# Kernel optimization log

Hardware: AMD Instinct MI355X
Metric: run time of the kernel (lower is better)

The kernel has to match this reference:

```python
import jax, jax.numpy as jnp
import numpy as np

N_NODES = 50000
N_EDGES = 800000
NUM_GRAPHS = 512
NEG_SLOPE = 0.2  # PyG GATv2Conv default negative_slope


def setup_inputs() -> dict:
    key = jax.random.key(0)
    ks = jax.random.split(key, 16)
    F_in, H = 128, 2
    C1, C2, NC = 32, 16, 6
    x = jax.random.normal(ks[0], (N_NODES, F_in), dtype=jnp.float32)
    edge_index = jax.random.randint(ks[1], (2, N_EDGES), 0, N_NODES, dtype=jnp.int64)
    batch = jnp.sort(jax.random.randint(ks[2], (N_NODES,), 0, NUM_GRAPHS, dtype=jnp.int64))
    s = lambda fan_in: 1.0 / np.sqrt(fan_in)
    return {
        "x": x, "edge_index": edge_index, "batch": batch,
        # conv1: in=128 -> heads=2, out=32 (concat 64)
        "Wl1": jax.random.normal(ks[3], (F_in, H * C1), jnp.float32) * s(F_in),
        "bl1": jnp.zeros((H * C1,), jnp.float32),
        "Wr1": jax.random.normal(ks[4], (F_in, H * C1), jnp.float32) * s(F_in),
        "att1": jax.random.normal(ks[5], (H, C1), jnp.float32) * s(C1),
        "b1": jnp.zeros((H * C1,), jnp.float32),
        # conv2: in=64 -> heads=2, out=16 (concat 32)
        "Wl2": jax.random.normal(ks[6], (H * C1, H * C2), jnp.float32) * s(H * C1),
        "bl2": jnp.zeros((H * C2,), jnp.float32),
        "Wr2": jax.random.normal(ks[7], (H * C1, H * C2), jnp.float32) * s(H * C1),
        "att2": jax.random.normal(ks[8], (H, C2), jnp.float32) * s(C2),
        "b2": jnp.zeros((H * C2,), jnp.float32),
        # fc: 32 -> 6
        "Wfc": jax.random.normal(ks[9], (H * C2, NC), jnp.float32) * s(H * C2),
        "bfc": jnp.zeros((NC,), jnp.float32),
    }


def _gatv2_conv(x, src, dst, Wl, bl, Wr, att, bias):
    """PyG GATv2Conv (concat heads, add_self_loops already applied to src/dst)."""
    H, C = att.shape
    N = x.shape[0]
    xl = (x @ Wl + bl).reshape(N, H, C)  # source/message transform
    xr = (x @ Wr).reshape(N, H, C)       # target transform
    e = jax.nn.leaky_relu(xl[src] + xr[dst], NEG_SLOPE)  # [E,H,C]
    score = jnp.einsum('ehc,hc->eh', e, att)             # [E,H]
    # segment softmax over edges sharing the same destination node
    smax = jax.ops.segment_max(score, dst, num_segments=N)      # [N,H]
    ex = jnp.exp(score - smax[dst])
    denom = jax.ops.segment_sum(ex, dst, num_segments=N)        # [N,H]
    alpha = ex / denom[dst]                                     # [E,H]
    out = jax.ops.segment_sum(alpha[:, :, None] * xl[src], dst, num_segments=N)
    return out.reshape(N, H * C) + bias


def reference(x, edge_index, batch, Wl1, bl1, Wr1, att1, b1,
              Wl2, bl2, Wr2, att2, b2, Wfc, bfc):
    N = x.shape[0]
    loops = jnp.arange(N, dtype=edge_index.dtype)
    src = jnp.concatenate([edge_index[0], loops])  # add_self_loops=True
    dst = jnp.concatenate([edge_index[1], loops])
    h = jax.nn.elu(_gatv2_conv(x, src, dst, Wl1, bl1, Wr1, att1, b1))
    h = jax.nn.elu(_gatv2_conv(h, src, dst, Wl2, bl2, Wr2, att2, b2))
    # global mean pool over graphs
    sums = jax.ops.segment_sum(h, batch, num_segments=NUM_GRAPHS)
    cnt = jax.ops.segment_sum(jnp.ones((N,), h.dtype), batch, num_segments=NUM_GRAPHS)
    pooled = sums / jnp.maximum(cnt, 1.0)[:, None]
    return jax.nn.log_softmax(pooled @ Wfc + bfc, axis=1)
```

## Files before the change

kernel.cpp:

```cpp
#include <hip/hip_runtime.h>
#include <math.h>

#define N_NODES 50000
#define N_EDGES 800000
#define NUM_GRAPHS 512
#define NEG_SLOPE 0.2f
#define LOG_MD 6
#define ROWCAP 63
#define NBKT 196
#define NPART 200
#define EPB_PART 4000

typedef unsigned short ushort_t;
typedef unsigned int   uint_t;
typedef __attribute__((ext_vector_type(4))) float f32x4;
typedef __attribute__((ext_vector_type(8))) short s16x8;

__device__ __forceinline__ ushort_t f2bf(float f) {
    union { float f; uint_t u; } v; v.f = f;
    uint_t u = v.u;
    return (ushort_t)((u + 0x7fffu + ((u >> 16) & 1u)) >> 16);
}

__global__ void hist_k(const int* __restrict__ ei_dst, int* __restrict__ bucket_cnt,
                       float* __restrict__ gz) {
    __shared__ int h[NBKT];
    const int tid = threadIdx.x;
    for (int i = tid; i < NBKT; i += 256) h[i] = 0;
    int gt = blockIdx.x * 256 + tid;
    if (gt < NUM_GRAPHS * 33) gz[gt] = 0.f;
    __syncthreads();
    const int base = blockIdx.x * EPB_PART;
    for (int i = tid; i < EPB_PART; i += 256)
        atomicAdd(&h[ei_dst[base + i] >> 8], 1);
    __syncthreads();
    for (int i = tid; i < NBKT; i += 256)
        if (h[i]) atomicAdd(&bucket_cnt[i], h[i]);
}

__global__ void bscan_k(const int* __restrict__ bucket_cnt,
                        int* __restrict__ bucket_off, int* __restrict__ bucket_cur) {
    __shared__ int s[256];
    int tid = threadIdx.x;
    s[tid] = (tid < NBKT) ? bucket_cnt[tid] : 0;
    __syncthreads();
    for (int off = 1; off < 256; off <<= 1) {
        int v = (tid >= off) ? s[tid - off] : 0;
        __syncthreads();
        s[tid] += v;
        __syncthreads();
    }
    if (tid < NBKT) {
        int excl = (tid == 0) ? 0 : s[tid - 1];
        bucket_off[tid] = excl;
        bucket_cur[tid] = excl;
    }
}

__global__ void __launch_bounds__(256) part_k(const int* __restrict__ ei,
                                              int* __restrict__ bucket_cur,
                                              int2* __restrict__ binned) {
    __shared__ int2 ebuf[EPB_PART];
    __shared__ int2 sbuf[EPB_PART];
    __shared__ int hist[NBKT], loff[NBKT], rk[NBKT], gbase[NBKT];
    __shared__ int s2[256];
    const int tid = threadIdx.x;
    for (int i = tid; i < NBKT; i += 256) { hist[i] = 0; rk[i] = 0; }
    __syncthreads();
    const int base = blockIdx.x * EPB_PART;
    for (int i = tid; i < EPB_PART; i += 256) {
        int s = ei[base + i];
        int d = ei[N_EDGES + base + i];
        ebuf[i] = make_int2(s, d);
        atomicAdd(&hist[d >> 8], 1);
    }
    __syncthreads();
    s2[tid] = (tid < NBKT) ? hist[tid] : 0;
    __syncthreads();
    for (int off = 1; off < 256; off <<= 1) {
        int v = (tid >= off) ? s2[tid - off] : 0;
        __syncthreads();
        s2[tid] += v;
        __syncthreads();
    }
    if (tid < NBKT) {
        loff[tid] = (tid == 0) ? 0 : s2[tid - 1];
        gbase[tid] = hist[tid] ? atomicAdd(&bucket_cur[tid], hist[tid]) : 0;
    }
    __syncthreads();
    for (int i = tid; i < EPB_PART; i += 256) {
        int2 e = ebuf[i];
        int b = e.y >> 8;
        int r = atomicAdd(&rk[b], 1);
        sbuf[loff[b] + r] = e;
    }
    __syncthreads();
    for (int i = tid; i < EPB_PART; i += 256) {
        int2 e = sbuf[i];
        int b = e.y >> 8;
        binned[gbase[b] + (i - loff[b])] = e;
    }
}

__global__ void __launch_bounds__(256) build_k(const int* __restrict__ bucket_off,
                                               const int2* __restrict__ binned,
                                               int* __restrict__ col) {
    __shared__ int win[256 * ROWCAP];
    __shared__ int cnt[256];
    const int tid = threadIdx.x;
    for (int i = tid; i < 256 * ROWCAP; i += 256) win[i] = 0;
    if (tid < 256) cnt[tid] = 0;
    __syncthreads();
    const int b = blockIdx.x;
    const int beg = bucket_off[b];
    const int end = (b == NBKT - 1) ? N_EDGES : bucket_off[b + 1];
    for (int i = beg + tid; i < end; i += 256) {
        int2 e = binned[i];
        int row = e.y & 255;
        int c = atomicAdd(&cnt[row], 1);
        if (c < ROWCAP) win[row * ROWCAP + c] = e.x;
    }
    __syncthreads();
    const int n0 = b << 8;
    const int nrows = min(256, N_NODES - n0);
    int* dst = col + ((size_t)n0 << LOG_MD);
    for (int i = tid; i < nrows * 64; i += 256) {
        int row = i >> 6, s = i & 63;
        dst[i] = (s == 63) ? min(cnt[row], ROWCAP) : win[row * ROWCAP + s];
    }
}

__global__ void prep_bt_k(const float* __restrict__ Wl, const float* __restrict__ Wr,
                          ushort_t* __restrict__ Bt) {
    int gid = blockIdx.x * 256 + threadIdx.x;
    int j = gid >> 7, k = gid & 127;
    float v = (j < 64) ? Wl[k * 64 + j] : Wr[k * 64 + (j - 64)];
    Bt[j * 128 + k] = f2bf(v);
}

__global__ void __launch_bounds__(256) linear1_mfma_k(
        const float* __restrict__ x, const ushort_t* __restrict__ Bt,
        const float* __restrict__ bl,
        float* __restrict__ xl, float* __restrict__ xr) {
    __shared__ ushort_t bts[128 * 136];
    const int tid = threadIdx.x;
    {
        const uint_t* src = (const uint_t*)Bt;
        uint_t* dst = (uint_t*)bts;
        for (int i = tid; i < 8192; i += 256) {
            int row = i >> 6, pos = i & 63;
            dst[row * 68 + pos] = src[i];
        }
    }
    __syncthreads();
    const int lane = tid & 63;
    const int wv = tid >> 6;
    const int q = lane >> 4, m = lane & 15;
    const int n0w = blockIdx.x * 64 + wv * 16;
    const int rowA = min(n0w + m, N_NODES - 1);
    const float* xrow = x + (size_t)rowA * 128;

    f32x4 acc[8];
    #pragma unroll
    for (int t = 0; t < 8; ++t) acc[t] = (f32x4){0.f, 0.f, 0.f, 0.f};

    #pragma unroll
    for (int ks = 0; ks < 4; ++ks) {
        const int k0 = ks * 32 + q * 8;
        float4 a0 = *(const float4*)(xrow + k0);
        float4 a1 = *(const float4*)(xrow + k0 + 4);
        s16x8 af;
        af[0] = (short)f2bf(a0.x); af[1] = (short)f2bf(a0.y);
        af[2] = (short)f2bf(a0.z); af[3] = (short)f2bf(a0.w);
        af[4] = (short)f2bf(a1.x); af[5] = (short)f2bf(a1.y);
        af[6] = (short)f2bf(a1.z); af[7] = (short)f2bf(a1.w);
        #pragma unroll
        for (int t = 0; t < 8; ++t) {
            const s16x8 bf = *(const s16x8*)(bts + (t * 16 + m) * 136 + k0);
            acc[t] = __builtin_amdgcn_mfma_f32_16x16x32_bf16(af, bf, acc[t], 0, 0, 0);
        }
    }
    #pragma unroll
    for (int t = 0; t < 8; ++t) {
        int j = t * 16 + m;
        float bias = (t < 4) ? bl[j] : 0.f;
        #pragma unroll
        for (int r = 0; r < 4; ++r) {
            int n = n0w + q * 4 + r;
            if (n < N_NODES) {
                if (t < 4) xl[(size_t)n * 64 + j] = acc[t][r] + bias;
                else       xr[(size_t)n * 64 + (j - 64)] = acc[t][r];
            }
        }
    }
}

template<int FIN, int FOUT, int NPB, int KC>
__global__ void __launch_bounds__(256) node_linear2_k(
        const float* __restrict__ x,
        const float* __restrict__ Wl, const float* __restrict__ bl,
        const float* __restrict__ Wr,
        float* __restrict__ xl, float* __restrict__ xr) {
    const int GROUPS = 256 / FOUT;
    const int NPG = NPB / GROUPS;
    __shared__ float xs[NPB * FIN];
    __shared__ float wls[KC * FOUT];
    __shared__ float wrs[KC * FOUT];
    const int tid = threadIdx.x;
    const int n0_blk = blockIdx.x * NPB;
    const int nodes_here = min(NPB, N_NODES - n0_blk);

    const float4* xv = (const float4*)(x + (size_t)n0_blk * FIN);
    const int total4 = nodes_here * FIN / 4;
    for (int i = tid; i < total4; i += 256) ((float4*)xs)[i] = xv[i];

    const int j = tid % FOUT;
    const int g = tid / FOUT;
    float al[NPG], ar[NPG];
    const float blj = bl[j];
    #pragma unroll
    for (int i = 0; i < NPG; ++i) { al[i] = blj; ar[i] = 0.f; }

    const float* xbase = xs + (size_t)g * NPG * FIN;
    for (int kc = 0; kc < FIN; kc += KC) {
        __syncthreads();
        const int CH4 = KC * FOUT / 4;
        const float4* wl4p = (const float4*)(Wl + (size_t)kc * FOUT);
        const float4* wr4p = (const float4*)(Wr + (size_t)kc * FOUT);
        for (int i = tid; i < CH4; i += 256) {
            ((float4*)wls)[i] = wl4p[i];
            ((float4*)wrs)[i] = wr4p[i];
        }
        __syncthreads();
        for (int k = 0; k < KC; k += 4) {
            float wl0 = wls[(k + 0) * FOUT + j], wl1 = wls[(k + 1) * FOUT + j];
            float wl2 = wls[(k + 2) * FOUT + j], wl3 = wls[(k + 3) * FOUT + j];
            float wr0 = wrs[(k + 0) * FOUT + j], wr1 = wrs[(k + 1) * FOUT + j];
            float wr2 = wrs[(k + 2) * FOUT + j], wr3 = wrs[(k + 3) * FOUT + j];
            #pragma unroll
            for (int i = 0; i < NPG; ++i) {
                float4 v = *(const float4*)(xbase + i * FIN + kc + k);
                al[i] = fmaf(v.x, wl0, fmaf(v.y, wl1, fmaf(v.z, wl2, fmaf(v.w, wl3, al[i]))));
                ar[i] = fmaf(v.x, wr0, fmaf(v.y, wr1, fmaf(v.z, wr2, fmaf(v.w, wr3, ar[i]))));
            }
        }
    }
    const int nbase = n0_blk + g * NPG;
    #pragma unroll
    for (int i = 0; i < NPG; ++i) {
        int n = nbase + i;
        if (n < N_NODES) {
            xl[(size_t)n * FOUT + j] = al[i];
            xr[(size_t)n * FOUT + j] = ar[i];
        }
    }
}

template<int C2, int LPN, int HEADL>
__global__ void gat_conv_k(const int* __restrict__ col,
                           const float4* __restrict__ xl4, const float4* __restrict__ xr4,
                           const float* __restrict__ att, const float* __restrict__ b,
                           float* __restrict__ out) {
    const int NPW = 64 / LPN;
    const int V4  = C2 / 4;
    int wave = (blockIdx.x * blockDim.x + threadIdx.x) >> 6;
    int lane = threadIdx.x & 63;
    int slot = lane / LPN;
    int c4   = lane % LPN;
    int n = wave * NPW + slot;
    const bool nvalid = (n < N_NODES);
    const int nn = nvalid ? n : (N_NODES - 1);

    const float4 xr_c  = xr4[(size_t)nn * V4 + c4];
    const float4 att_c = ((const float4*)att)[c4];
    const float4 b_c   = ((const float4*)b)[c4];

    const int start = nn << LOG_MD;
    const int dg    = nvalid ? min(col[start + 63], ROWCAP) : 0;

    float4 xs4 = xl4[(size_t)nn * V4 + c4];
    float den;
    float4 acc;
    {
        float z0 = xs4.x + xr_c.x; z0 = (z0 >= 0.f) ? z0 : NEG_SLOPE * z0;
        float z1 = xs4.y + xr_c.y; z1 = (z1 >= 0.f) ? z1 : NEG_SLOPE * z1;
        float z2 = xs4.z + xr_c.z; z2 = (z2 >= 0.f) ? z2 : NEG_SLOPE * z2;
        float z3 = xs4.w + xr_c.w; z3 = (z3 >= 0.f) ? z3 : NEG_SLOPE * z3;
        float p = fmaf(z0, att_c.x, fmaf(z1, att_c.y, fmaf(z2, att_c.z, z3 * att_c.w)));
        #pragma unroll
        for (int off = HEADL / 2; off > 0; off >>= 1)
            p += __shfl_xor(p, off, 64);
        float ex = __expf(fminf(p, 80.f));
        den = ex;
        acc.x = ex * xs4.x; acc.y = ex * xs4.y; acc.z = ex * xs4.z; acc.w = ex * xs4.w;
    }

    int mdg = dg;
    #pragma unroll
    for (int off = 32; off > 0; off >>= 1) mdg = max(mdg, __shfl_xor(mdg, off, 64));

    float4 cur = xl4[(size_t)col[start] * V4 + c4];
    for (int k = 0; k < mdg; ++k) {
        float4 x4 = cur;
        if (k + 1 < mdg) {
            int kk = min(k + 1, dg - 1);
            if (kk < 0) kk = 0;
            int sn = col[start + kk];
            cur = xl4[(size_t)sn * V4 + c4];
        }
        float z0 = x4.x + xr_c.x; z0 = (z0 >= 0.f) ? z0 : NEG_SLOPE * z0;
        float z1 = x4.y + xr_c.y; z1 = (z1 >= 0.f) ? z1 : NEG_SLOPE * z1;
        float z2 = x4.z + xr_c.z; z2 = (z2 >= 0.f) ? z2 : NEG_SLOPE * z2;
        float z3 = x4.w + xr_c.w; z3 = (z3 >= 0.f) ? z3 : NEG_SLOPE * z3;
        float p = fmaf(z0, att_c.x, fmaf(z1, att_c.y, fmaf(z2, att_c.z, z3 * att_c.w)));
        #pragma unroll
        for (int off = HEADL / 2; off > 0; off >>= 1)
            p += __shfl_xor(p, off, 64);
        float ex = (k < dg) ? __expf(fminf(p, 80.f)) : 0.f;
        den += ex;
        acc.x = fmaf(ex, x4.x, acc.x);
        acc.y = fmaf(ex, x4.y, acc.y);
        acc.z = fmaf(ex, x4.z, acc.z);
        acc.w = fmaf(ex, x4.w, acc.w);
    }
    if (nvalid) {
        float inv = 1.f / den;
        float4 o;
        o.x = fmaf(acc.x, inv, b_c.x); o.x = (o.x > 0.f) ? o.x : (__expf(o.x) - 1.f);
        o.y = fmaf(acc.y, inv, b_c.y); o.y = (o.y > 0.f) ? o.y : (__expf(o.y) - 1.f);
        o.z = fmaf(acc.z, inv, b_c.z); o.z = (o.z > 0.f) ? o.z : (__expf(o.z) - 1.f);
        o.w = fmaf(acc.w, inv, b_c.w); o.w = (o.w > 0.f) ? o.w : (__expf(o.w) - 1.f);
        ((float4*)out)[(size_t)n * V4 + c4] = o;
    }
}

__global__ void pool_k(const float* __restrict__ h2, const int* __restrict__ batch,
                       float* __restrict__ gsum, float* __restrict__ gcnt) {
    const int NCH = (N_NODES + 7) / 8;
    int t = blockIdx.x * blockDim.x + threadIdx.x;
    if (t >= NCH * 32) return;
    int c = t & 31;
    int n0 = (t >> 5) * 8;
    int nend = min(n0 + 8, N_NODES);
    int curb = batch[n0];
    float s = 0.f, cnt = 0.f;
    for (int n = n0; n < nend; ++n) {
        int bb = batch[n];
        if (bb != curb) {
            atomicAdd(gsum + (size_t)curb * 32 + c, s);
            if (c == 0) atomicAdd(gcnt + curb, cnt);
            s = 0.f; cnt = 0.f; curb = bb;
        }
        s += h2[(size_t)n * 32 + c];
        cnt += 1.f;
    }
    atomicAdd(gsum + (size_t)curb * 32 + c, s);
    if (c == 0) atomicAdd(gcnt + curb, cnt);
}

__global__ void head_k(const float* __restrict__ gsum, const float* __restrict__ gcnt,
                       const float* __restrict__ Wfc, const float* __restrict__ bfc,
                       float* __restrict__ out) {
    int gph = blockIdx.x * blockDim.x + threadIdx.x;
    if (gph >= NUM_GRAPHS) return;
    float inv = 1.f / fmaxf(gcnt[gph], 1.f);
    float logits[6];
    #pragma unroll
    for (int j = 0; j < 6; ++j) logits[j] = bfc[j];
    for (int k = 0; k < 32; ++k) {
        float p = gsum[(size_t)gph * 32 + k] * inv;
        #pragma unroll
        for (int j = 0; j < 6; ++j) logits[j] = fmaf(p, Wfc[k * 6 + j], logits[j]);
    }
    float m = logits[0];
    #pragma unroll
    for (int j = 1; j < 6; ++j) m = fmaxf(m, logits[j]);
    float ssum = 0.f;
    #pragma unroll
    for (int j = 0; j < 6; ++j) ssum += expf(logits[j] - m);
    float lse = m + logf(ssum);
    #pragma unroll
    for (int j = 0; j < 6; ++j) out[(size_t)gph * 6 + j] = logits[j] - lse;
}

extern "C" void kernel_launch(void* const* d_in, const int* in_sizes, int n_in,
                              void* d_out, int out_size, void* d_ws, size_t ws_size,
                              hipStream_t stream) {
    const float* x    = (const float*)d_in[0];
    const int*   ei   = (const int*)d_in[1];
    const int*   batch= (const int*)d_in[2];
    const float* Wl1  = (const float*)d_in[3];
    const float* bl1  = (const float*)d_in[4];
    const float* Wr1  = (const float*)d_in[5];
    const float* att1 = (const float*)d_in[6];
    const float* b1   = (const float*)d_in[7];
    const float* Wl2  = (const float*)d_in[8];
    const float* bl2  = (const float*)d_in[9];
    const float* Wr2  = (const float*)d_in[10];
    const float* att2 = (const float*)d_in[11];
    const float* b2   = (const float*)d_in[12];
    const float* Wfc  = (const float*)d_in[13];
    const float* bfc  = (const float*)d_in[14];
    float* out = (float*)d_out;

    char* wsp = (char*)d_ws;
    float* xl1  = (float*)wsp; wsp += (size_t)N_NODES * 64 * 4;
    float* xr1  = (float*)wsp; wsp += (size_t)N_NODES * 64 * 4;
    float* h1   = (float*)wsp; wsp += (size_t)N_NODES * 64 * 4;
    float* xl2  = (float*)wsp; wsp += (size_t)N_NODES * 32 * 4;
    float* xr2  = (float*)wsp; wsp += (size_t)N_NODES * 32 * 4;
    float* h2   = (float*)wsp; wsp += (size_t)N_NODES * 32 * 4;
    float* gsum = (float*)wsp; wsp += (size_t)NUM_GRAPHS * 32 * 4;
    float* gcnt = (float*)wsp; wsp += (size_t)NUM_GRAPHS * 4;
    int* col    = (int*)wsp; wsp += ((size_t)N_NODES << LOG_MD) * 4;
    int* bucket_cnt = (int*)wsp; wsp += NBKT * 4;
    int* bucket_off = (int*)wsp; wsp += NBKT * 4;
    int* bucket_cur = (int*)wsp; wsp += NBKT * 4;
    ushort_t* Bt = (ushort_t*)wsp; wsp += 128 * 128 * 2;
    int2* binned = (int2*)h1;

    const int TB = 256;

    hipMemsetAsync(bucket_cnt, 0, NBKT * sizeof(int), stream);
    prep_bt_k<<<64, 256, 0, stream>>>(Wl1, Wr1, Bt);
    hist_k<<<NPART, 256, 0, stream>>>(ei + N_EDGES, bucket_cnt, gsum);
    bscan_k<<<1, 256, 0, stream>>>(bucket_cnt, bucket_off, bucket_cur);
    part_k<<<NPART, 256, 0, stream>>>(ei, bucket_cur, binned);
    build_k<<<NBKT, 256, 0, stream>>>(bucket_off, binned, col);

    linear1_mfma_k<<<(N_NODES + 63) / 64, 256, 0, stream>>>(x, Bt, bl1, xl1, xr1);
    {
        int waves = (N_NODES + 3) / 4;
        gat_conv_k<64, 16, 8><<<(waves + 3) / 4, 256, 0, stream>>>(
            col, (const float4*)xl1, (const float4*)xr1, att1, b1, h1);
    }

    node_linear2_k<64, 32, 64, 32><<<(N_NODES + 63) / 64, 256, 0, stream>>>(
        h1, Wl2, bl2, Wr2, xl2, xr2);
    {
        int waves = (N_NODES + 7) / 8;
        gat_conv_k<32, 8, 4><<<(waves + 3) / 4, 256, 0, stream>>>(
            col, (const float4*)xl2, (const float4*)xr2, att2, b2, h2);
    }

    pool_k<<<(((N_NODES + 7) / 8) * 32 + TB - 1) / TB, TB, 0, stream>>>(h2, batch, gsum, gcnt);
    head_k<<<(NUM_GRAPHS + TB - 1) / TB, TB, 0, stream>>>(gsum, gcnt, Wfc, bfc, out);
}
```

Before: 250.9 us.

## Store node features in bf16 and use MFMA for second linear layer

Intermediate node features (xl, xr, h1 for both layers) are now stored as bf16 instead of fp32, which halves the bytes moved by the gather-heavy attention kernels. Each lane in the attention kernel now handles 8 channels instead of 4, so more nodes fit per wave. The scalar FMA second linear layer is replaced with a bf16 MFMA kernel whose transposed weights are prepared alongside layer one's. This lowers the precision of the features and of the attention inputs, which may change accuracy.

```diff
diff --git a/kernel.cpp b/kernel.cpp
--- a/kernel.cpp
+++ b/kernel.cpp
@@ -22,6 +22,14 @@
     return (ushort_t)((u + 0x7fffu + ((u >> 16) & 1u)) >> 16);
 }
 
+__device__ __forceinline__ void unpack8(const ushort_t* p, float* f) {
+    uint4 u = *(const uint4*)p;
+    f[0] = __uint_as_float(u.x << 16); f[1] = __uint_as_float(u.x & 0xffff0000u);
+    f[2] = __uint_as_float(u.y << 16); f[3] = __uint_as_float(u.y & 0xffff0000u);
+    f[4] = __uint_as_float(u.z << 16); f[5] = __uint_as_float(u.z & 0xffff0000u);
+    f[6] = __uint_as_float(u.w << 16); f[7] = __uint_as_float(u.w & 0xffff0000u);
+}
+
 __global__ void hist_k(const int* __restrict__ ei_dst, int* __restrict__ bucket_cnt,
                        float* __restrict__ gz) {
     __shared__ int h[NBKT];
@@ -130,18 +138,26 @@
     }
 }
 
-__global__ void prep_bt_k(const float* __restrict__ Wl, const float* __restrict__ Wr,
-                          ushort_t* __restrict__ Bt) {
+__global__ void prep_bt_k(const float* __restrict__ Wl1, const float* __restrict__ Wr1,
+                          const float* __restrict__ Wl2, const float* __restrict__ Wr2,
+                          ushort_t* __restrict__ Bt1, ushort_t* __restrict__ Bt2) {
     int gid = blockIdx.x * 256 + threadIdx.x;
-    int j = gid >> 7, k = gid & 127;
-    float v = (j < 64) ? Wl[k * 64 + j] : Wr[k * 64 + (j - 64)];
-    Bt[j * 128 + k] = f2bf(v);
+    if (gid < 16384) {
+        int j = gid >> 7, k = gid & 127;
+        float v = (j < 64) ? Wl1[k * 64 + j] : Wr1[k * 64 + (j - 64)];
+        Bt1[gid] = f2bf(v);
+    } else if (gid < 16384 + 4096) {
+        int g = gid - 16384;
+        int j = g >> 6, k = g & 63;
+        float v = (j < 32) ? Wl2[k * 32 + j] : Wr2[k * 32 + (j - 32)];
+        Bt2[g] = f2bf(v);
+    }
 }
 
 __global__ void __launch_bounds__(256) linear1_mfma_k(
         const float* __restrict__ x, const ushort_t* __restrict__ Bt,
         const float* __restrict__ bl,
-        float* __restrict__ xl, float* __restrict__ xr) {
+        ushort_t* __restrict__ xl, ushort_t* __restrict__ xr) {
     __shared__ ushort_t bts[128 * 136];
     const int tid = threadIdx.x;
     {
@@ -188,149 +204,162 @@
         for (int r = 0; r < 4; ++r) {
             int n = n0w + q * 4 + r;
             if (n < N_NODES) {
-                if (t < 4) xl[(size_t)n * 64 + j] = acc[t][r] + bias;
-                else       xr[(size_t)n * 64 + (j - 64)] = acc[t][r];
+                if (t < 4) xl[(size_t)n * 64 + j] = f2bf(acc[t][r] + bias);
+                else       xr[(size_t)n * 64 + (j - 64)] = f2bf(acc[t][r]);
             }
         }
     }
 }
 
-template<int FIN, int FOUT, int NPB, int KC>
-__global__ void __launch_bounds__(256) node_linear2_k(
-        const float* __restrict__ x,
-        const float* __restrict__ Wl, const float* __restrict__ bl,
-        const float* __restrict__ Wr,
-        float* __restrict__ xl, float* __restrict__ xr) {
-    const int GROUPS = 256 / FOUT;
-    const int NPG = NPB / GROUPS;
-    __shared__ float xs[NPB * FIN];
-    __shared__ float wls[KC * FOUT];
-    __shared__ float wrs[KC * FOUT];
+__global__ void __launch_bounds__(256) linear2_mfma_k(
+        const ushort_t* __restrict__ h1, const ushort_t* __restrict__ Bt2,
+        const float* __restrict__ bl2,
+        ushort_t* __restrict__ xl2, ushort_t* __restrict__ xr2) {
+    __shared__ ushort_t bts[64 * 72];
     const int tid = threadIdx.x;
-    const int n0_blk = blockIdx.x * NPB;
-    const int nodes_here = min(NPB, N_NODES - n0_blk);
-
-    const float4* xv = (const float4*)(x + (size_t)n0_blk * FIN);
-    const int total4 = nodes_here * FIN / 4;
-    for (int i = tid; i < total4; i += 256) ((float4*)xs)[i] = xv[i];
-
-    const int j = tid % FOUT;
-    const int g = tid / FOUT;
-    float al[NPG], ar[NPG];
-    const float blj = bl[j];
-    #pragma unroll
-    for (int i = 0; i < NPG; ++i) { al[i] = blj; ar[i] = 0.f; }
-
-    const float* xbase = xs + (size_t)g * NPG * FIN;
-    for (int kc = 0; kc < FIN; kc += KC) {
-        __syncthreads();
-        const int CH4 = KC * FOUT / 4;
-        const float4* wl4p = (const float4*)(Wl + (size_t)kc * FOUT);
-        const float4* wr4p = (const float4*)(Wr + (size_t)kc * FOUT);
-        for (int i = tid; i < CH4; i += 256) {
-            ((float4*)wls)[i] = wl4p[i];
-            ((float4*)wrs)[i] = wr4p[i];
-        }
-        __syncthreads();
-        for (int k = 0; k < KC; k += 4) {
-            float wl0 = wls[(k + 0) * FOUT + j], wl1 = wls[(k + 1) * FOUT + j];
-            float wl2 = wls[(k + 2) * FOUT + j], wl3 = wls[(k + 3) * FOUT + j];
-            float wr0 = wrs[(k + 0) * FOUT + j], wr1 = wrs[(k + 1) * FOUT + j];
-            float wr2 = wrs[(k + 2) * FOUT + j], wr3 = wrs[(k + 3) * FOUT + j];
-            #pragma unroll
-            for (int i = 0; i < NPG; ++i) {
-                float4 v = *(const float4*)(xbase + i * FIN + kc + k);
-                al[i] = fmaf(v.x, wl0, fmaf(v.y, wl1, fmaf(v.z, wl2, fmaf(v.w, wl3, al[i]))));
-                ar[i] = fmaf(v.x, wr0, fmaf(v.y, wr1, fmaf(v.z, wr2, fmaf(v.w, wr3, ar[i]))));
+    {
+        const uint_t* src = (const uint_t*)Bt2;
+        uint_t* dst = (uint_t*)bts;
+        for (int i = tid; i < 2048; i += 256) {
+            int row = i >> 5, pos = i & 31;
+            dst[row * 36 + pos] = src[i];
+        }
+    }
+    __syncthreads();
+    const int lane = tid & 63;
+    const int wv = tid >> 6;
+    const int q = lane >> 4, m = lane & 15;
+    const int n0w = blockIdx.x * 64 + wv * 16;
+    const int rowA = min(n0w + m, N_NODES - 1);
+    const ushort_t* hrow = h1 + (size_t)rowA * 64;
+
+    f32x4 acc[4];
+    #pragma unroll
+    for (int t = 0; t < 4; ++t) acc[t] = (f32x4){0.f, 0.f, 0.f, 0.f};
+
+    #pragma unroll
+    for (int ks = 0; ks < 2; ++ks) {
+        const int k0 = ks * 32 + q * 8;
+        const s16x8 af = *(const s16x8*)(hrow + k0);
+        #pragma unroll
+        for (int t = 0; t < 4; ++t) {
+            const s16x8 bf = *(const s16x8*)(bts + (t * 16 + m) * 72 + k0);
+            acc[t] = __builtin_amdgcn_mfma_f32_16x16x32_bf16(af, bf, acc[t], 0, 0, 0);
+        }
+    }
+    #pragma unroll
+    for (int t = 0; t < 4; ++t) {
+        int j = t * 16 + m;
+        float bias = (t < 2) ? bl2[j] : 0.f;
+        #pragma unroll
+        for (int r = 0; r < 4; ++r) {
+            int n = n0w + q * 4 + r;
+            if (n < N_NODES) {
+                if (t < 2) xl2[(size_t)n * 32 + j] = f2bf(acc[t][r] + bias);
+                else       xr2[(size_t)n * 32 + (j - 32)] = f2bf(acc[t][r]);
             }
         }
     }
-    const int nbase = n0_blk + g * NPG;
-    #pragma unroll
-    for (int i = 0; i < NPG; ++i) {
-        int n = nbase + i;
-        if (n < N_NODES) {
-            xl[(size_t)n * FOUT + j] = al[i];
-            xr[(size_t)n * FOUT + j] = ar[i];
-        }
-    }
-}
-
-template<int C2, int LPN, int HEADL>
-__global__ void gat_conv_k(const int* __restrict__ col,
-                           const float4* __restrict__ xl4, const float4* __restrict__ xr4,
-                           const float* __restrict__ att, const float* __restrict__ b,
-                           float* __restrict__ out) {
+}
+
+template<int C2, int LPN, int HEADL, bool OUT_BF16>
+__global__ void __launch_bounds__(256) gat_conv_k(
+        const int* __restrict__ col,
+        const ushort_t* __restrict__ xl, const ushort_t* __restrict__ xr,
+        const float* __restrict__ att, const float* __restrict__ b,
+        void* __restrict__ outp) {
     const int NPW = 64 / LPN;
-    const int V4  = C2 / 4;
     int wave = (blockIdx.x * blockDim.x + threadIdx.x) >> 6;
     int lane = threadIdx.x & 63;
     int slot = lane / LPN;
-    int c4   = lane % LPN;
+    int c8   = lane % LPN;
     int n = wave * NPW + slot;
     const bool nvalid = (n < N_NODES);
     const int nn = nvalid ? n : (N_NODES - 1);
 
-    const float4 xr_c  = xr4[(size_t)nn * V4 + c4];
-    const float4 att_c = ((const float4*)att)[c4];
-    const float4 b_c   = ((const float4*)b)[c4];
+    float xrv[8], attv[8], bv[8];
+    unpack8(xr + (size_t)nn * C2 + c8 * 8, xrv);
+    *(float4*)(attv)     = ((const float4*)att)[c8 * 2];
+    *(float4*)(attv + 4) = ((const float4*)att)[c8 * 2 + 1];
+    *(float4*)(bv)       = ((const float4*)b)[c8 * 2];
+    *(float4*)(bv + 4)   = ((const float4*)b)[c8 * 2 + 1];
 
     const int start = nn << LOG_MD;
-    const int dg    = nvalid ? min(col[start + 63], ROWCAP) : 0;
-
-    float4 xs4 = xl4[(size_t)nn * V4 + c4];
-    float den;
-    float4 acc;
+    const int dg = nvalid ? min(col[start + 63], ROWCAP) : 0;
+
+    float den, acc[8];
     {
-        float z0 = xs4.x + xr_c.x; z0 = (z0 >= 0.f) ? z0 : NEG_SLOPE * z0;
-        float z1 = xs4.y + xr_c.y; z1 = (z1 >= 0.f) ? z1 : NEG_SLOPE * z1;
-        float z2 = xs4.z + xr_c.z; z2 = (z2 >= 0.f) ? z2 : NEG_SLOPE * z2;
-        float z3 = xs4.w + xr_c.w; z3 = (z3 >= 0.f) ? z3 : NEG_SLOPE * z3;
-        float p = fmaf(z0, att_c.x, fmaf(z1, att_c.y, fmaf(z2, att_c.z, z3 * att_c.w)));
+        float xsv[8];
+        unpack8(xl + (size_t)nn * C2 + c8 * 8, xsv);
+        float p = 0.f;
+        #pragma unroll
+        for (int i = 0; i < 8; ++i) {
+            float z = xsv[i] + xrv[i];
+            z = (z >= 0.f) ? z : NEG_SLOPE * z;
+            p = fmaf(z, attv[i], p);
+        }
         #pragma unroll
         for (int off = HEADL / 2; off > 0; off >>= 1)
             p += __shfl_xor(p, off, 64);
         float ex = __expf(fminf(p, 80.f));
         den = ex;
-        acc.x = ex * xs4.x; acc.y = ex * xs4.y; acc.z = ex * xs4.z; acc.w = ex * xs4.w;
+        #pragma unroll
+        for (int i = 0; i < 8; ++i) acc[i] = ex * xsv[i];
     }
 
     int mdg = dg;
     #pragma unroll
     for (int off = 32; off > 0; off >>= 1) mdg = max(mdg, __shfl_xor(mdg, off, 64));
 
-    float4 cur = xl4[(size_t)col[start] * V4 + c4];
+    uint4 raw = *(const uint4*)(xl + (size_t)col[start] * C2 + c8 * 8);
     for (int k = 0; k < mdg; ++k) {
-        float4 x4 = cur;
+        uint4 cu = raw;
         if (k + 1 < mdg) {
             int kk = min(k + 1, dg - 1);
             if (kk < 0) kk = 0;
             int sn = col[start + kk];
-            cur = xl4[(size_t)sn * V4 + c4];
-        }
-        float z0 = x4.x + xr_c.x; z0 = (z0 >= 0.f) ? z0 : NEG_SLOPE * z0;
-        float z1 = x4.y + xr_c.y; z1 = (z1 >= 0.f) ? z1 : NEG_SLOPE * z1;
-        float z2 = x4.z + xr_c.z; z2 = (z2 >= 0.f) ? z2 : NEG_SLOPE * z2;
-        float z3 = x4.w + xr_c.w; z3 = (z3 >= 0.f) ? z3 : NEG_SLOPE * z3;
-        float p = fmaf(z0, att_c.x, fmaf(z1, att_c.y, fmaf(z2, att_c.z, z3 * att_c.w)));
+            raw = *(const uint4*)(xl + (size_t)sn * C2 + c8 * 8);
+        }
+        float xv[8];
+        xv[0] = __uint_as_float(cu.x << 16); xv[1] = __uint_as_float(cu.x & 0xffff0000u);
+        xv[2] = __uint_as_float(cu.y << 16); xv[3] = __uint_as_float(cu.y & 0xffff0000u);
+        xv[4] = __uint_as_float(cu.z << 16); xv[5] = __uint_as_float(cu.z & 0xffff0000u);
+        xv[6] = __uint_as_float(cu.w << 16); xv[7] = __uint_as_float(cu.w & 0xffff0000u);
+        float p = 0.f;
+        #pragma unroll
+        for (int i = 0; i < 8; ++i) {
+            float z = xv[i] + xrv[i];
+            z = (z >= 0.f) ? z : NEG_SLOPE * z;
+            p = fmaf(z, attv[i], p);
+        }
         #pragma unroll
         for (int off = HEADL / 2; off > 0; off >>= 1)
             p += __shfl_xor(p, off, 64);
         float ex = (k < dg) ? __expf(fminf(p, 80.f)) : 0.f;
         den += ex;
-        acc.x = fmaf(ex, x4.x, acc.x);
-        acc.y = fmaf(ex, x4.y, acc.y);
-        acc.z = fmaf(ex, x4.z, acc.z);
-        acc.w = fmaf(ex, x4.w, acc.w);
+        #pragma unroll
+        for (int i = 0; i < 8; ++i) acc[i] = fmaf(ex, xv[i], acc[i]);
     }
     if (nvalid) {
         float inv = 1.f / den;
-        float4 o;
-        o.x = fmaf(acc.x, inv, b_c.x); o.x = (o.x > 0.f) ? o.x : (__expf(o.x) - 1.f);
-        o.y = fmaf(acc.y, inv, b_c.y); o.y = (o.y > 0.f) ? o.y : (__expf(o.y) - 1.f);
-        o.z = fmaf(acc.z, inv, b_c.z); o.z = (o.z > 0.f) ? o.z : (__expf(o.z) - 1.f);
-        o.w = fmaf(acc.w, inv, b_c.w); o.w = (o.w > 0.f) ? o.w : (__expf(o.w) - 1.f);
-        ((float4*)out)[(size_t)n * V4 + c4] = o;
+        float o[8];
+        #pragma unroll
+        for (int i = 0; i < 8; ++i) {
+            float v = fmaf(acc[i], inv, bv[i]);
+            o[i] = (v > 0.f) ? v : (__expf(v) - 1.f);
+        }
+        if (OUT_BF16) {
+            uint4 u;
+            u.x = ((uint_t)f2bf(o[1]) << 16) | f2bf(o[0]);
+            u.y = ((uint_t)f2bf(o[3]) << 16) | f2bf(o[2]);
+            u.z = ((uint_t)f2bf(o[5]) << 16) | f2bf(o[4]);
+            u.w = ((uint_t)f2bf(o[7]) << 16) | f2bf(o[6]);
+            ((uint4*)outp)[(size_t)n * (C2 / 8) + c8] = u;
+        } else {
+            float4* op = (float4*)outp;
+            op[(size_t)n * (C2 / 4) + c8 * 2]     = *(float4*)o;
+            op[(size_t)n * (C2 / 4) + c8 * 2 + 1] = *(float4*)(o + 4);
+        }
     }
 }
 
@@ -404,11 +433,11 @@
     float* out = (float*)d_out;
 
     char* wsp = (char*)d_ws;
-    float* xl1  = (float*)wsp; wsp += (size_t)N_NODES * 64 * 4;
-    float* xr1  = (float*)wsp; wsp += (size_t)N_NODES * 64 * 4;
-    float* h1   = (float*)wsp; wsp += (size_t)N_NODES * 64 * 4;
-    float* xl2  = (float*)wsp; wsp += (size_t)N_NODES * 32 * 4;
-    float* xr2  = (float*)wsp; wsp += (size_t)N_NODES * 32 * 4;
+    ushort_t* xl1 = (ushort_t*)wsp; wsp += (size_t)N_NODES * 64 * 2;
+    ushort_t* xr1 = (ushort_t*)wsp; wsp += (size_t)N_NODES * 64 * 2;
+    ushort_t* h1  = (ushort_t*)wsp; wsp += (size_t)N_NODES * 64 * 2;
+    ushort_t* xl2 = (ushort_t*)wsp; wsp += (size_t)N_NODES * 32 * 2;
+    ushort_t* xr2 = (ushort_t*)wsp; wsp += (size_t)N_NODES * 32 * 2;
     float* h2   = (float*)wsp; wsp += (size_t)N_NODES * 32 * 4;
     float* gsum = (float*)wsp; wsp += (size_t)NUM_GRAPHS * 32 * 4;
     float* gcnt = (float*)wsp; wsp += (size_t)NUM_GRAPHS * 4;
@@ -416,31 +445,32 @@
     int* bucket_cnt = (int*)wsp; wsp += NBKT * 4;
     int* bucket_off = (int*)wsp; wsp += NBKT * 4;
     int* bucket_cur = (int*)wsp; wsp += NBKT * 4;
-    ushort_t* Bt = (ushort_t*)wsp; wsp += 128 * 128 * 2;
+    wsp += 16 - ((size_t)wsp & 15);
+    ushort_t* Bt1 = (ushort_t*)wsp; wsp += 128 * 128 * 2;
+    ushort_t* Bt2 = (ushort_t*)wsp; wsp += 64 * 64 * 2;
     int2* binned = (int2*)h1;
 
     const int TB = 256;
 
     hipMemsetAsync(bucket_cnt, 0, NBKT * sizeof(int), stream);
-    prep_bt_k<<<64, 256, 0, stream>>>(Wl1, Wr1, Bt);
+    prep_bt_k<<<80, 256, 0, stream>>>(Wl1, Wr1, Wl2, Wr2, Bt1, Bt2);
     hist_k<<<NPART, 256, 0, stream>>>(ei + N_EDGES, bucket_cnt, gsum);
     bscan_k<<<1, 256, 0, stream>>>(bucket_cnt, bucket_off, bucket_cur);
     part_k<<<NPART, 256, 0, stream>>>(ei, bucket_cur, binned);
     build_k<<<NBKT, 256, 0, stream>>>(bucket_off, binned, col);
 
-    linear1_mfma_k<<<(N_NODES + 63) / 64, 256, 0, stream>>>(x, Bt, bl1, xl1, xr1);
-    {
-        int waves = (N_NODES + 3) / 4;
-        gat_conv_k<64, 16, 8><<<(waves + 3) / 4, 256, 0, stream>>>(
-            col, (const float4*)xl1, (const float4*)xr1, att1, b1, h1);
-    }
-
-    node_linear2_k<64, 32, 64, 32><<<(N_NODES + 63) / 64, 256, 0, stream>>>(
-        h1, Wl2, bl2, Wr2, xl2, xr2);
+    linear1_mfma_k<<<(N_NODES + 63) / 64, 256, 0, stream>>>(x, Bt1, bl1, xl1, xr1);
     {
         int waves = (N_NODES + 7) / 8;
-        gat_conv_k<32, 8, 4><<<(waves + 3) / 4, 256, 0, stream>>>(
-            col, (const float4*)xl2, (const float4*)xr2, att2, b2, h2);
+        gat_conv_k<64, 8, 4, true><<<(waves + 3) / 4, 256, 0, stream>>>(
+            col, xl1, xr1, att1, b1, h1);
+    }
+
+    linear2_mfma_k<<<(N_NODES + 63) / 64, 256, 0, stream>>>(h1, Bt2, bl2, xl2, xr2);
+    {
+        int waves = (N_NODES + 15) / 16;
+        gat_conv_k<32, 4, 2, false><<<(waves + 3) / 4, 256, 0, stream>>>(
+            col, xl2, xr2, att2, b2, h2);
     }
 
     pool_k<<<(((N_NODES + 7) / 8) * 32 + TB - 1) / TB, TB, 0, stream>>>(h2, batch, gsum, gcnt);
```

After: 217.4 us. 13.3% less time.
